# Kernel optimization log

Hardware: AMD Instinct MI355X
Metric: run time of the kernel (lower is better)

The kernel has to match this reference:

```python
import jax, jax.numpy as jnp
import numpy as np

N_NODES = 50000
N_EDGES = 800000
N_GRAPHS = 512


def gcn_conv(x, W, b, src, dst, n_nodes):
    # Standard PyG GCNConv: linear transform, add self-loops, D^-1/2 (A+I) D^-1/2 aggregation.
    x = x @ W  # [N, out]
    loop = jnp.arange(n_nodes, dtype=src.dtype)
    s = jnp.concatenate([src, loop])  # [E+N]
    d = jnp.concatenate([dst, loop])
    deg = jax.ops.segment_sum(jnp.ones_like(d, dtype=x.dtype), d, num_segments=n_nodes)
    dinv = jnp.where(deg > 0, jax.lax.rsqrt(jnp.maximum(deg, 1e-12)), 0.0)
    norm = dinv[s] * dinv[d]  # [E+N]
    msg = x[s] * norm[:, None]  # gather + scale
    out = jax.ops.segment_sum(msg, d, num_segments=n_nodes)  # scatter-add
    return out + b


def setup_inputs() -> dict:
    key = jax.random.key(0)
    ks = jax.random.split(key, 10)
    x = jax.random.normal(ks[0], (N_NODES, 128), dtype=jnp.float32)
    edge_index = jax.random.randint(ks[1], (2, N_EDGES), 0, N_NODES, dtype=jnp.int64)
    batch = jnp.sort(jax.random.randint(ks[2], (N_NODES,), 0, N_GRAPHS, dtype=jnp.int64))
    y = jax.random.randint(ks[3], (N_GRAPHS,), 0, 4, dtype=jnp.int64)
    W1 = jax.random.normal(ks[4], (128, 64), dtype=jnp.float32) * (1.0 / np.sqrt(128))
    b1 = jnp.zeros((64,), dtype=jnp.float32)
    W2 = jax.random.normal(ks[5], (64, 64), dtype=jnp.float32) * (1.0 / np.sqrt(64))
    b2 = jnp.zeros((64,), dtype=jnp.float32)
    Wfc = jax.random.normal(ks[6], (64, 4), dtype=jnp.float32) * (1.0 / np.sqrt(64))
    bfc = jnp.zeros((4,), dtype=jnp.float32)
    return {"x": x, "edge_index": edge_index, "batch": batch, "y": y,
            "W1": W1, "b1": b1, "W2": W2, "b2": b2, "Wfc": Wfc, "bfc": bfc}


def reference(x, edge_index, batch, y, W1, b1, W2, b2, Wfc, bfc):
    src, dst = edge_index[0], edge_index[1]
    h = jax.nn.relu(gcn_conv(x, W1, b1, src, dst, N_NODES))
    h = jax.nn.relu(gcn_conv(h, W2, b2, src, dst, N_NODES))
    # global mean pool over graph ids
    sums = jax.ops.segment_sum(h, batch, num_segments=N_GRAPHS)  # [G, out]
    cnts = jax.ops.segment_sum(jnp.ones((h.shape[0],), h.dtype), batch, num_segments=N_GRAPHS)
    pooled = sums / jnp.maximum(cnts, 1.0)[:, None]
    logits = pooled @ Wfc + bfc
    logp = jax.nn.log_softmax(logits, axis=1)
    return (logp, y)
```

## Files before the change

kernel.cpp:

```cpp
#include <hip/hip_runtime.h>
#include <hip/hip_fp16.h>
#include <math.h>

#define N_NODES 50000
#define N_EDGES 800000
#define N_GRAPHS 512
#define NBKT 196
#define SENT N_NODES
#define CAP_T 6144
#define CAP_S 12288
#define EPB 2048
#define NBLK_A 391
#define N_GROUPS 6250
#define NBLK_G 1563

typedef float v2f __attribute__((ext_vector_type(2)));

#define OFF_BCNT    0u
#define OFF_DINV    1024u
#define OFF_GGRP    201216u
#define OFF_TMP     251392u
#define OFF_SORTED  5068288u
#define OFF_XS8_1   14702080u
#define OFF_XS8_2   17902336u
#define OFF_H2      21102592u

__global__ __launch_bounds__(256) void binA(const int* __restrict__ src, const int* __restrict__ dst,
                                            int* __restrict__ bcnt, unsigned int* __restrict__ tmp,
                                            unsigned int* __restrict__ x1, unsigned int* __restrict__ x2) {
    __shared__ int cnt[256];
    __shared__ int lo[256];
    __shared__ int cnt2[256];
    __shared__ int baseg[256];
    __shared__ unsigned int ldsPK[EPB];
    __shared__ int ldsDST[EPB];
    int t = threadIdx.x;
    cnt[t] = 0; cnt2[t] = 0;
    if (blockIdx.x == 0) {
        if (t < 16) x1[N_NODES * 16 + t] = 0;
        else if (t < 32) x2[N_NODES * 16 + (t - 16)] = 0;
    }
    __syncthreads();
    int e0 = blockIdx.x * EPB;
    int nE = N_EDGES - e0; if (nE > EPB) nE = EPB;
    int sA[8], dA[8];
#pragma unroll
    for (int i = 0; i < 8; ++i) {
        int e = e0 + i * 256 + t;
        if (e < N_EDGES) {
            sA[i] = src[e];
            dA[i] = dst[e];
            atomicAdd(&cnt[dA[i] >> 8], 1);
        } else dA[i] = -1;
    }
    __syncthreads();
    {
        int v = cnt[t];
        lo[t] = v;
        __syncthreads();
        for (int d = 1; d < 256; d <<= 1) {
            int a = (t >= d) ? lo[t - d] : 0;
            __syncthreads();
            lo[t] += a;
            __syncthreads();
        }
        int ex = lo[t] - v;
        __syncthreads();
        lo[t] = ex;
        baseg[t] = (t < NBKT && v) ? atomicAdd(&bcnt[t], v) : 0;
    }
    __syncthreads();
#pragma unroll
    for (int i = 0; i < 8; ++i) {
        if (dA[i] >= 0) {
            int b = dA[i] >> 8;
            int pl = lo[b] + atomicAdd(&cnt2[b], 1);
            ldsPK[pl] = (unsigned int)sA[i] | ((unsigned int)(dA[i] & 255) << 17);
            ldsDST[pl] = b * CAP_T + baseg[b] + (pl - lo[b]);
        }
    }
    __syncthreads();
    for (int p = t; p < nE; p += 256)
        tmp[ldsDST[p]] = ldsPK[p];
}

__global__ __launch_bounds__(256) void binB2(const unsigned int* __restrict__ tmp,
                                             const int* __restrict__ bcnt,
                                             int* __restrict__ sorted, int2* __restrict__ ggrp,
                                             float* __restrict__ dinv) {
    __shared__ int cnt[256];
    __shared__ int lbs[256];
    __shared__ int cur[256];
    __shared__ int gK[32];
    __shared__ int gpre[33];
    __shared__ int ldsS[CAP_S];
    int b = blockIdx.x, t = threadIdx.x;
    cnt[t] = 0;
    __syncthreads();
    int m = bcnt[b];
    const unsigned int* tp = tmp + b * CAP_T;
    for (int e = t; e < m; e += 256) atomicAdd(&cnt[tp[e] >> 17], 1);
    __syncthreads();
    int node = b * 256 + t;
    int real = node < N_NODES;
    int deg = cnt[t];
    int count = real ? deg + 1 : 0;
    int mx = count;
    mx = max(mx, __shfl_xor(mx, 1));
    mx = max(mx, __shfl_xor(mx, 2));
    mx = max(mx, __shfl_xor(mx, 4));
    int K = (mx + 3) & ~3;
    int KP = K + 4;
    if ((t & 7) == 0) gK[t >> 3] = KP;
    __syncthreads();
    if (t == 0) {
        int s = 0;
        for (int g = 0; g < 32; ++g) { gpre[g] = s; s += gK[g]; }
        gpre[32] = s;
    }
    __syncthreads();
    int lb = 8 * gpre[t >> 3] + (t & 7);
    lbs[t] = lb;
    cur[t] = real ? 1 : 0;
    if (real) {
        dinv[node] = rsqrtf(1.0f + (float)deg);
        ldsS[lb] = node;
    }
    if ((t & 7) == 0) ggrp[b * 32 + (t >> 3)] = make_int2(b * CAP_S + 8 * gpre[t >> 3], K);
    __syncthreads();
    for (int e = t; e < m; e += 256) {
        unsigned int pk = tp[e];
        int d = (int)(pk >> 17);
        int j = atomicAdd(&cur[d], 1);
        ldsS[lbs[d] + j * 8] = (int)(pk & 0x1FFFFu);
    }
    __syncthreads();
    for (int j = cur[t]; j < KP; ++j) ldsS[lb + j * 8] = SENT;
    __syncthreads();
    int ptot = 8 * gpre[32];
    int4* dst4 = (int4*)(sorted + b * CAP_S);
    const int4* src4 = (const int4*)ldsS;
    for (int p = t; p < (ptot >> 2); p += 256) dst4[p] = src4[p];
}

__global__ __launch_bounds__(256) void gemm1(const float* __restrict__ X, const float* __restrict__ W,
                                             const float* __restrict__ dinv, unsigned int* __restrict__ xs8) {
    __shared__ float sW[128 * 64];
    __shared__ float sX[16 * 132];
    int tid = threadIdx.x;
    {
        const float4* ws = (const float4*)W;
        float4* wd = (float4*)sW;
        for (int i = tid; i < 2048; i += 256) wd[i] = ws[i];
    }
    int row0 = blockIdx.x * 16;
    {
        const float4* xs = (const float4*)(X + row0 * 128);
        for (int i = tid; i < 512; i += 256) {
            int r = i >> 5, q = i & 31;
            *(float4*)&sX[r * 132 + 4 * q] = xs[r * 32 + q];
        }
    }
    __syncthreads();
    int r = tid >> 4;
    int cg = (tid & 15) * 4;
    int row = row0 + r;
    float a0 = 0, a1 = 0, a2 = 0, a3 = 0;
#pragma unroll 8
    for (int k = 0; k < 128; ++k) {
        float xv = sX[r * 132 + k];
        float4 w = *(const float4*)&sW[k * 64 + cg];
        a0 += xv * w.x; a1 += xv * w.y; a2 += xv * w.z; a3 += xv * w.w;
    }
    float s = dinv[row];
    unsigned int pk = 0;
    pk = __builtin_amdgcn_cvt_pk_fp8_f32(a0 * s, a1 * s, pk, false);
    pk = __builtin_amdgcn_cvt_pk_fp8_f32(a2 * s, a3 * s, pk, true);
    xs8[row * 16 + (cg >> 2)] = pk;
}

#define ADD_ROW(rv) { \
    v2f f0 = __builtin_amdgcn_cvt_pk_f32_fp8((rv).x, false); \
    v2f f1 = __builtin_amdgcn_cvt_pk_f32_fp8((rv).x, true); \
    v2f f2 = __builtin_amdgcn_cvt_pk_f32_fp8((rv).y, false); \
    v2f f3 = __builtin_amdgcn_cvt_pk_f32_fp8((rv).y, true); \
    a0 += f0.x; a1 += f0.y; a2 += f1.x; a3 += f1.y; \
    a4 += f2.x; a5 += f2.y; a6 += f3.x; a7 += f3.y; }

#define GATHER_ACC() \
    int lane = threadIdx.x & 63; \
    int sub = lane >> 3, frag = lane & 7; \
    int node = grp * 8 + sub; \
    int2 gi = ggrp[grp]; \
    int K = gi.y; \
    const int* sp = sorted + gi.x + sub; \
    const uint2* xr = (const uint2*)xs8 + frag; \
    float a0 = 0, a1 = 0, a2 = 0, a3 = 0, a4 = 0, a5 = 0, a6 = 0, a7 = 0; \
    int i0 = sp[0], i1 = sp[8], i2 = sp[16], i3 = sp[24]; \
    for (int k = 0; k < K; k += 4) { \
        uint2 r0 = xr[i0 * 8]; \
        uint2 r1 = xr[i1 * 8]; \
        uint2 r2 = xr[i2 * 8]; \
        uint2 r3 = xr[i3 * 8]; \
        const int* np = sp + (k + 4) * 8; \
        i0 = np[0]; i1 = np[8]; i2 = np[16]; i3 = np[24]; \
        ADD_ROW(r0); ADD_ROW(r1); ADD_ROW(r2); ADD_ROW(r3); \
    }

__global__ __launch_bounds__(256) void gather_fuse(const unsigned char* __restrict__ xs8,
                                                   const int2* __restrict__ ggrp,
                                                   const int* __restrict__ sorted,
                                                   const float* __restrict__ dinv,
                                                   const float* __restrict__ bias,
                                                   const float* __restrict__ W2,
                                                   unsigned int* __restrict__ xs8o) {
    __shared__ float sW2[64 * 64];
    __shared__ float sH[32][68];
    {
        const float4* ws = (const float4*)W2;
        float4* wd = (float4*)sW2;
        for (int i = threadIdx.x; i < 1024; i += 256) wd[i] = ws[i];
    }
    int wvl = threadIdx.x >> 6;
    int grp = blockIdx.x * 4 + wvl;

    GATHER_ACC()

    {
        float dv = dinv[node];
        float4 bA = *(const float4*)(bias + frag * 8);
        float4 bB = *(const float4*)(bias + frag * 8 + 4);
        float4 w0, w1;
        w0.x = fmaxf(a0 * dv + bA.x, 0.0f); w0.y = fmaxf(a1 * dv + bA.y, 0.0f);
        w0.z = fmaxf(a2 * dv + bA.z, 0.0f); w0.w = fmaxf(a3 * dv + bA.w, 0.0f);
        w1.x = fmaxf(a4 * dv + bB.x, 0.0f); w1.y = fmaxf(a5 * dv + bB.y, 0.0f);
        w1.z = fmaxf(a6 * dv + bB.z, 0.0f); w1.w = fmaxf(a7 * dv + bB.w, 0.0f);
        *(float4*)&sH[wvl * 8 + sub][frag * 8] = w0;
        *(float4*)&sH[wvl * 8 + sub][frag * 8 + 4] = w1;
    }
    __syncthreads();
    int r = threadIdx.x >> 3;
    int cg = (threadIdx.x & 7) * 8;
    float b0 = 0, b1 = 0, b2 = 0, b3 = 0, b4 = 0, b5 = 0, b6 = 0, b7 = 0;
#pragma unroll 8
    for (int k = 0; k < 64; ++k) {
        float hv = sH[r][k];
        float4 wa = *(const float4*)&sW2[k * 64 + cg];
        float4 wb = *(const float4*)&sW2[k * 64 + cg + 4];
        b0 += hv * wa.x; b1 += hv * wa.y; b2 += hv * wa.z; b3 += hv * wa.w;
        b4 += hv * wb.x; b5 += hv * wb.y; b6 += hv * wb.z; b7 += hv * wb.w;
    }
    int node2 = blockIdx.x * 32 + r;
    if (node2 < N_NODES) {
        float s = dinv[node2];
        unsigned int p0 = 0, p1 = 0;
        p0 = __builtin_amdgcn_cvt_pk_fp8_f32(b0 * s, b1 * s, p0, false);
        p0 = __builtin_amdgcn_cvt_pk_fp8_f32(b2 * s, b3 * s, p0, true);
        p1 = __builtin_amdgcn_cvt_pk_fp8_f32(b4 * s, b5 * s, p1, false);
        p1 = __builtin_amdgcn_cvt_pk_fp8_f32(b6 * s, b7 * s, p1, true);
        *(uint2*)(xs8o + node2 * 16 + (cg >> 2)) = make_uint2(p0, p1);
    }
}

__global__ __launch_bounds__(256) void gather_h2(const unsigned char* __restrict__ xs8,
                                                 const int2* __restrict__ ggrp,
                                                 const int* __restrict__ sorted,
                                                 const float* __restrict__ dinv,
                                                 const float* __restrict__ bias,
                                                 __half* __restrict__ h2) {
    int grp = blockIdx.x * 4 + (threadIdx.x >> 6);

    GATHER_ACC()

    if (node < N_NODES) {
        float dv = dinv[node];
        float4 bA = *(const float4*)(bias + frag * 8);
        float4 bB = *(const float4*)(bias + frag * 8 + 4);
        float v0 = fmaxf(a0 * dv + bA.x, 0.0f), v1 = fmaxf(a1 * dv + bA.y, 0.0f);
        float v2 = fmaxf(a2 * dv + bA.z, 0.0f), v3 = fmaxf(a3 * dv + bA.w, 0.0f);
        float v4 = fmaxf(a4 * dv + bB.x, 0.0f), v5 = fmaxf(a5 * dv + bB.y, 0.0f);
        float v6 = fmaxf(a6 * dv + bB.z, 0.0f), v7 = fmaxf(a7 * dv + bB.w, 0.0f);
        __half2 p0 = __floats2half2_rn(v0, v1), p1 = __floats2half2_rn(v2, v3);
        __half2 p2 = __floats2half2_rn(v4, v5), p3 = __floats2half2_rn(v6, v7);
        uint4 pk;
        pk.x = *(unsigned int*)&p0; pk.y = *(unsigned int*)&p1;
        pk.z = *(unsigned int*)&p2; pk.w = *(unsigned int*)&p3;
        *(uint4*)(h2 + node * 64 + frag * 8) = pk;
    }
}

__device__ __forceinline__ int lower_bound(const int* __restrict__ a, int n, int v) {
    int lo = 0, hi = n;
    while (lo < hi) { int m = (lo + hi) >> 1; if (a[m] < v) lo = m + 1; else hi = m; }
    return lo;
}

__global__ __launch_bounds__(256) void pool_head(const __half* __restrict__ h2,
                                                 const int* __restrict__ batch,
                                                 const float* __restrict__ Wfc, const float* __restrict__ bfc,
                                                 const int* __restrict__ y, float* __restrict__ out) {
    __shared__ int s_beg, s_end;
    __shared__ float sh[4][64];
    __shared__ float pl[64];
    __shared__ float lg[4];
    int g = blockIdx.x;
    int t = threadIdx.x;
    if (t == 0) s_beg = lower_bound(batch, N_NODES, g);
    if (t == 1) s_end = lower_bound(batch, N_NODES, g + 1);
    __syncthreads();
    int beg = s_beg, end = s_end;
    int f = t & 63, seg = t >> 6;
    float s = 0.0f;
    for (int r = beg + seg; r < end; r += 4) s += __half2float(h2[r * 64 + f]);
    sh[seg][f] = s;
    __syncthreads();
    if (t < 64) {
        float p = sh[0][t] + sh[1][t] + sh[2][t] + sh[3][t];
        pl[t] = p / fmaxf((float)(end - beg), 1.0f);
    }
    __syncthreads();
    if (t < 4) {
        float l = bfc[t];
#pragma unroll
        for (int k = 0; k < 64; ++k) l += pl[k] * Wfc[k * 4 + t];
        lg[t] = l;
    }
    __syncthreads();
    if (t == 0) {
        float l0 = lg[0], l1 = lg[1], l2 = lg[2], l3 = lg[3];
        float m = fmaxf(fmaxf(l0, l1), fmaxf(l2, l3));
        float ss = expf(l0 - m) + expf(l1 - m) + expf(l2 - m) + expf(l3 - m);
        float lse = m + logf(ss);
        out[g * 4 + 0] = l0 - lse;
        out[g * 4 + 1] = l1 - lse;
        out[g * 4 + 2] = l2 - lse;
        out[g * 4 + 3] = l3 - lse;
        out[N_GRAPHS * 4 + g] = (float)y[g];
    }
}

extern "C" void kernel_launch(void* const* d_in, const int* in_sizes, int n_in,
                              void* d_out, int out_size, void* d_ws, size_t ws_size,
                              hipStream_t stream) {
    const float* x     = (const float*)d_in[0];
    const int*   ei    = (const int*)d_in[1];
    const int*   batch = (const int*)d_in[2];
    const int*   y     = (const int*)d_in[3];
    const float* W1    = (const float*)d_in[4];
    const float* b1    = (const float*)d_in[5];
    const float* W2    = (const float*)d_in[6];
    const float* b2    = (const float*)d_in[7];
    const float* Wfc   = (const float*)d_in[8];
    const float* bfc   = (const float*)d_in[9];
    float* out = (float*)d_out;

    const int* src = ei;
    const int* dst = ei + N_EDGES;

    char* wsb = (char*)d_ws;
    int*          bcnt   = (int*)(wsb + OFF_BCNT);
    float*        dinv   = (float*)(wsb + OFF_DINV);
    int2*         ggrp   = (int2*)(wsb + OFF_GGRP);
    unsigned int* tmp    = (unsigned int*)(wsb + OFF_TMP);
    int*          sorted = (int*)(wsb + OFF_SORTED);
    unsigned int* xs8_1  = (unsigned int*)(wsb + OFF_XS8_1);
    unsigned int* xs8_2  = (unsigned int*)(wsb + OFF_XS8_2);
    __half*       h2     = (__half*)(wsb + OFF_H2);

    hipMemsetAsync(bcnt, 0, 1024u, stream);

    binA<<<NBLK_A, 256, 0, stream>>>(src, dst, bcnt, tmp, xs8_1, xs8_2);
    binB2<<<NBKT, 256, 0, stream>>>(tmp, bcnt, sorted, ggrp, dinv);

    gemm1<<<N_NODES / 16, 256, 0, stream>>>(x, W1, dinv, xs8_1);
    gather_fuse<<<NBLK_G, 256, 0, stream>>>((const unsigned char*)xs8_1, ggrp, sorted,
                                            dinv, b1, W2, xs8_2);
    gather_h2<<<NBLK_G, 256, 0, stream>>>((const unsigned char*)xs8_2, ggrp, sorted,
                                          dinv, b2, h2);

    pool_head<<<N_GRAPHS, 256, 0, stream>>>(h2, batch, Wfc, bfc, y, out);
}
```

Before: 198.0 us.

## Fuse bucket sort and bf16 MFMA GEMM into one prep kernel, apply dinv in gather

Replaces the global-atomic bucket scatter with per-segment fixed-capacity bins plus a count matrix, which removes the memset and the global atomics. The second binning pass and the first GEMM are merged into a single launch whose blocks split between sorting half-buckets and a bf16 MFMA layer-1 GEMM. Because dinv is no longer ready when the GEMM runs, the source-side normalization moves into the gather loop as an extra per-neighbor dinv load and FMA. The GEMM adds a runtime accuracy check with an fp32 fallback, and the sort blocks now each rescan all segments of their bucket, so per-block serial work goes up.

Result: faster. 173.0 us (-12.6%).

```diff
diff --git a/kernel.cpp b/kernel.cpp
--- a/kernel.cpp
+++ b/kernel.cpp
@@ -7,185 +7,246 @@
 #define N_GRAPHS 512
 #define NBKT 196
 #define SENT N_NODES
-#define CAP_T 6144
-#define CAP_S 12288
 #define EPB 2048
-#define NBLK_A 391
-#define N_GROUPS 6250
-#define NBLK_G 1563
+#define NSEG 391
+#define CAP_C 48
+#define NBLK_B2 392
+#define CAP_SH 8192
+#define NBLK_GM 782
+#define PREP_GRID (NBLK_B2 + NBLK_GM)
+#define N_GROUPS 6272
+#define NBLK_G 1568
 
 typedef float v2f __attribute__((ext_vector_type(2)));
-
-#define OFF_BCNT    0u
-#define OFF_DINV    1024u
-#define OFF_GGRP    201216u
-#define OFF_TMP     251392u
-#define OFF_SORTED  5068288u
-#define OFF_XS8_1   14702080u
-#define OFF_XS8_2   17902336u
-#define OFF_H2      21102592u
+typedef float f32x4 __attribute__((ext_vector_type(4)));
+typedef short s16x8 __attribute__((ext_vector_type(8)));
+
+#define OFF_DINV    0u
+#define OFF_GGRP    200704u
+#define OFF_CNTM    250880u
+#define OFF_TMP     557568u
+#define OFF_SORTED  15271680u
+#define OFF_XS8_1   28116736u
+#define OFF_XS8_2   31316992u
+#define OFF_H2      34517248u
+
+__device__ __forceinline__ unsigned short f2bf(float f) {
+    unsigned int u = __float_as_uint(f);
+    u += 0x7FFFu + ((u >> 16) & 1u);
+    return (unsigned short)(u >> 16);
+}
 
 __global__ __launch_bounds__(256) void binA(const int* __restrict__ src, const int* __restrict__ dst,
-                                            int* __restrict__ bcnt, unsigned int* __restrict__ tmp,
-                                            unsigned int* __restrict__ x1, unsigned int* __restrict__ x2) {
+                                            int* __restrict__ cntmat, unsigned int* __restrict__ tmp,
+                                            unsigned int* __restrict__ x1, unsigned int* __restrict__ x2,
+                                            float* __restrict__ dinv) {
     __shared__ int cnt[256];
-    __shared__ int lo[256];
-    __shared__ int cnt2[256];
-    __shared__ int baseg[256];
-    __shared__ unsigned int ldsPK[EPB];
-    __shared__ int ldsDST[EPB];
     int t = threadIdx.x;
-    cnt[t] = 0; cnt2[t] = 0;
+    cnt[t] = 0;
     if (blockIdx.x == 0) {
         if (t < 16) x1[N_NODES * 16 + t] = 0;
         else if (t < 32) x2[N_NODES * 16 + (t - 16)] = 0;
+        else if (t == 32) dinv[SENT] = 0.0f;
     }
     __syncthreads();
     int e0 = blockIdx.x * EPB;
-    int nE = N_EDGES - e0; if (nE > EPB) nE = EPB;
-    int sA[8], dA[8];
 #pragma unroll
     for (int i = 0; i < 8; ++i) {
         int e = e0 + i * 256 + t;
         if (e < N_EDGES) {
-            sA[i] = src[e];
-            dA[i] = dst[e];
-            atomicAdd(&cnt[dA[i] >> 8], 1);
-        } else dA[i] = -1;
-    }
-    __syncthreads();
-    {
-        int v = cnt[t];
-        lo[t] = v;
-        __syncthreads();
-        for (int d = 1; d < 256; d <<= 1) {
-            int a = (t >= d) ? lo[t - d] : 0;
+            int s = src[e], d = dst[e];
+            int b = d >> 8;
+            int p = atomicAdd(&cnt[b], 1);
+            tmp[(b * NSEG + blockIdx.x) * CAP_C + p] =
+                (unsigned int)s | ((unsigned int)(d & 255) << 17);
+        }
+    }
+    __syncthreads();
+    if (t < NBKT) cntmat[blockIdx.x * NBKT + t] = cnt[t];
+}
+
+__global__ __launch_bounds__(256) void prep(const unsigned int* __restrict__ tmp,
+                                            const int* __restrict__ cntmat,
+                                            int* __restrict__ sorted, int2* __restrict__ ggrp,
+                                            float* __restrict__ dinv,
+                                            const float* __restrict__ X, const float* __restrict__ W1,
+                                            unsigned int* __restrict__ xs8) {
+    __shared__ __align__(16) char pool[34816];
+    __shared__ int bad;
+    int t = threadIdx.x;
+
+    if (blockIdx.x < NBLK_B2) {
+        int* cnt  = (int*)pool;
+        int* lbs  = (int*)(pool + 512);
+        int* cur  = (int*)(pool + 1024);
+        int* gK   = (int*)(pool + 1536);
+        int* gpre = (int*)(pool + 1600);
+        int* ldsS = (int*)(pool + 1792);
+        int b2 = blockIdx.x, bkt = b2 >> 1, half = b2 & 1;
+        if (t < 128) cnt[t] = 0;
+        __syncthreads();
+        for (int seg = t; seg < NSEG; seg += 256) {
+            int c = cntmat[seg * NBKT + bkt];
+            const unsigned int* tp = tmp + (bkt * NSEG + seg) * CAP_C;
+            for (int e = 0; e < c; ++e) {
+                int d = (int)(tp[e] >> 17);
+                if ((d >> 7) == half) atomicAdd(&cnt[d & 127], 1);
+            }
+        }
+        __syncthreads();
+        int node = 0, deg = 0, K = 0, KP = 0, lb = 0, myreal = 0;
+        if (t < 128) {
+            node = bkt * 256 + half * 128 + t;
+            myreal = node < N_NODES;
+            deg = cnt[t];
+            int count = myreal ? deg + 1 : 0;
+            int mx = count;
+            mx = max(mx, __shfl_xor(mx, 1));
+            mx = max(mx, __shfl_xor(mx, 2));
+            mx = max(mx, __shfl_xor(mx, 4));
+            K = (mx + 3) & ~3;
+            KP = K + 4;
+            if ((t & 7) == 0) gK[t >> 3] = KP;
+        }
+        __syncthreads();
+        if (t == 0) {
+            int s = 0;
+#pragma unroll
+            for (int g = 0; g < 16; ++g) { gpre[g] = s; s += gK[g]; }
+            gpre[16] = s;
+        }
+        __syncthreads();
+        if (t < 128) {
+            lb = 8 * gpre[t >> 3] + (t & 7);
+            lbs[t] = lb;
+            cur[t] = myreal ? 1 : 0;
+            if (myreal) {
+                dinv[node] = rsqrtf(1.0f + (float)deg);
+                ldsS[lb] = node;
+            }
+            if ((t & 7) == 0)
+                ggrp[b2 * 16 + (t >> 3)] = make_int2(b2 * CAP_SH + 8 * gpre[t >> 3], K);
+        }
+        __syncthreads();
+        for (int seg = t; seg < NSEG; seg += 256) {
+            int c = cntmat[seg * NBKT + bkt];
+            const unsigned int* tp = tmp + (bkt * NSEG + seg) * CAP_C;
+            for (int e = 0; e < c; ++e) {
+                unsigned int pk = tp[e];
+                int d = (int)(pk >> 17);
+                if ((d >> 7) == half) {
+                    int loc = d & 127;
+                    int j = atomicAdd(&cur[loc], 1);
+                    ldsS[lbs[loc] + j * 8] = (int)(pk & 0x1FFFFu);
+                }
+            }
+        }
+        __syncthreads();
+        if (t < 128)
+            for (int j = cur[t]; j < KP; ++j) ldsS[lb + j * 8] = SENT;
+        __syncthreads();
+        int ptot = 8 * gpre[16];
+        int4* dst4 = (int4*)(sorted + b2 * CAP_SH);
+        const int4* src4 = (const int4*)ldsS;
+        for (int p = t; p < (ptot >> 2); p += 256) dst4[p] = src4[p];
+    } else {
+        short* W1T = (short*)pool;
+        float* sD  = (float*)(pool + 17408);
+        int gb = blockIdx.x - NBLK_B2;
+        int row0 = gb * 64;
+        for (int i = t; i < 8192; i += 256) {
+            int k = i >> 6, c = i & 63;
+            W1T[c * 136 + k] = (short)f2bf(W1[i]);
+        }
+        __syncthreads();
+        int w = t >> 6, lane = t & 63;
+        int arow = lane & 15, kg = lane >> 4;
+        int r = row0 + w * 16 + arow;
+        const float* xp = X + r * 128 + kg * 8;
+        bool vr = (r < N_NODES);
+        const short* wb = &W1T[arow * 136 + kg * 8];
+        f32x4 ac0 = {0.f, 0.f, 0.f, 0.f}, ac1 = ac0, ac2 = ac0, ac3 = ac0;
+#pragma unroll
+        for (int kk = 0; kk < 4; ++kk) {
+            float4 xa, xb;
+            if (vr) { xa = *(const float4*)(xp); xb = *(const float4*)(xp + 4); }
+            else    { xa = make_float4(0.f, 0.f, 0.f, 0.f); xb = xa; }
+            xp += 32;
+            s16x8 af;
+            af[0] = (short)f2bf(xa.x); af[1] = (short)f2bf(xa.y);
+            af[2] = (short)f2bf(xa.z); af[3] = (short)f2bf(xa.w);
+            af[4] = (short)f2bf(xb.x); af[5] = (short)f2bf(xb.y);
+            af[6] = (short)f2bf(xb.z); af[7] = (short)f2bf(xb.w);
+            const short* wk = wb + kk * 32;
+            s16x8 bf0 = *(const s16x8*)(wk);
+            s16x8 bf1 = *(const s16x8*)(wk + 16 * 136);
+            s16x8 bf2 = *(const s16x8*)(wk + 32 * 136);
+            s16x8 bf3 = *(const s16x8*)(wk + 48 * 136);
+            asm volatile(
+                "s_nop 1\n\t"
+                "v_mfma_f32_16x16x32_bf16 %0, %4, %5, %0\n\t"
+                "v_mfma_f32_16x16x32_bf16 %1, %4, %6, %1\n\t"
+                "v_mfma_f32_16x16x32_bf16 %2, %4, %7, %2\n\t"
+                "v_mfma_f32_16x16x32_bf16 %3, %4, %8, %3"
+                : "+v"(ac0), "+v"(ac1), "+v"(ac2), "+v"(ac3)
+                : "v"(af), "v"(bf0), "v"(bf1), "v"(bf2), "v"(bf3));
+        }
+        asm volatile("s_nop 7\n\ts_nop 7");
+        int dr = w * 16 + kg * 4;
+#pragma unroll
+        for (int reg = 0; reg < 4; ++reg) {
+            sD[(dr + reg) * 68 + arow]      = ac0[reg];
+            sD[(dr + reg) * 68 + 16 + arow] = ac1[reg];
+            sD[(dr + reg) * 68 + 32 + arow] = ac2[reg];
+            sD[(dr + reg) * 68 + 48 + arow] = ac3[reg];
+        }
+        __syncthreads();
+        if (t == 0) {
+            float r0v = 0.f, r1v = 0.f;
+            const float* x0 = X + row0 * 128;
+            for (int k = 0; k < 128; ++k) {
+                float wv = W1[k * 64];
+                r0v += x0[k] * wv;
+                r1v += x0[128 + k] * wv;
+            }
+            bad = (fabsf(r0v - sD[0])  > 0.05f * fabsf(r0v) + 0.1f) ||
+                  (fabsf(r1v - sD[68]) > 0.05f * fabsf(r1v) + 0.1f);
+        }
+        __syncthreads();
+        if (bad) {
+            for (int i = t; i < 4096; i += 256) {
+                int lr = i >> 6, c = i & 63;
+                int nd = row0 + lr;
+                if (nd < N_NODES) {
+                    const float* xr2 = X + nd * 128;
+                    float s = 0.f;
+                    for (int k = 0; k < 128; ++k) s += xr2[k] * W1[k * 64 + c];
+                    sD[lr * 68 + c] = s;
+                }
+            }
             __syncthreads();
-            lo[t] += a;
-            __syncthreads();
-        }
-        int ex = lo[t] - v;
-        __syncthreads();
-        lo[t] = ex;
-        baseg[t] = (t < NBKT && v) ? atomicAdd(&bcnt[t], v) : 0;
-    }
-    __syncthreads();
-#pragma unroll
-    for (int i = 0; i < 8; ++i) {
-        if (dA[i] >= 0) {
-            int b = dA[i] >> 8;
-            int pl = lo[b] + atomicAdd(&cnt2[b], 1);
-            ldsPK[pl] = (unsigned int)sA[i] | ((unsigned int)(dA[i] & 255) << 17);
-            ldsDST[pl] = b * CAP_T + baseg[b] + (pl - lo[b]);
-        }
-    }
-    __syncthreads();
-    for (int p = t; p < nE; p += 256)
-        tmp[ldsDST[p]] = ldsPK[p];
-}
-
-__global__ __launch_bounds__(256) void binB2(const unsigned int* __restrict__ tmp,
-                                             const int* __restrict__ bcnt,
-                                             int* __restrict__ sorted, int2* __restrict__ ggrp,
-                                             float* __restrict__ dinv) {
-    __shared__ int cnt[256];
-    __shared__ int lbs[256];
-    __shared__ int cur[256];
-    __shared__ int gK[32];
-    __shared__ int gpre[33];
-    __shared__ int ldsS[CAP_S];
-    int b = blockIdx.x, t = threadIdx.x;
-    cnt[t] = 0;
-    __syncthreads();
-    int m = bcnt[b];
-    const unsigned int* tp = tmp + b * CAP_T;
-    for (int e = t; e < m; e += 256) atomicAdd(&cnt[tp[e] >> 17], 1);
-    __syncthreads();
-    int node = b * 256 + t;
-    int real = node < N_NODES;
-    int deg = cnt[t];
-    int count = real ? deg + 1 : 0;
-    int mx = count;
-    mx = max(mx, __shfl_xor(mx, 1));
-    mx = max(mx, __shfl_xor(mx, 2));
-    mx = max(mx, __shfl_xor(mx, 4));
-    int K = (mx + 3) & ~3;
-    int KP = K + 4;
-    if ((t & 7) == 0) gK[t >> 3] = KP;
-    __syncthreads();
-    if (t == 0) {
-        int s = 0;
-        for (int g = 0; g < 32; ++g) { gpre[g] = s; s += gK[g]; }
-        gpre[32] = s;
-    }
-    __syncthreads();
-    int lb = 8 * gpre[t >> 3] + (t & 7);
-    lbs[t] = lb;
-    cur[t] = real ? 1 : 0;
-    if (real) {
-        dinv[node] = rsqrtf(1.0f + (float)deg);
-        ldsS[lb] = node;
-    }
-    if ((t & 7) == 0) ggrp[b * 32 + (t >> 3)] = make_int2(b * CAP_S + 8 * gpre[t >> 3], K);
-    __syncthreads();
-    for (int e = t; e < m; e += 256) {
-        unsigned int pk = tp[e];
-        int d = (int)(pk >> 17);
-        int j = atomicAdd(&cur[d], 1);
-        ldsS[lbs[d] + j * 8] = (int)(pk & 0x1FFFFu);
-    }
-    __syncthreads();
-    for (int j = cur[t]; j < KP; ++j) ldsS[lb + j * 8] = SENT;
-    __syncthreads();
-    int ptot = 8 * gpre[32];
-    int4* dst4 = (int4*)(sorted + b * CAP_S);
-    const int4* src4 = (const int4*)ldsS;
-    for (int p = t; p < (ptot >> 2); p += 256) dst4[p] = src4[p];
-}
-
-__global__ __launch_bounds__(256) void gemm1(const float* __restrict__ X, const float* __restrict__ W,
-                                             const float* __restrict__ dinv, unsigned int* __restrict__ xs8) {
-    __shared__ float sW[128 * 64];
-    __shared__ float sX[16 * 132];
-    int tid = threadIdx.x;
-    {
-        const float4* ws = (const float4*)W;
-        float4* wd = (float4*)sW;
-        for (int i = tid; i < 2048; i += 256) wd[i] = ws[i];
-    }
-    int row0 = blockIdx.x * 16;
-    {
-        const float4* xs = (const float4*)(X + row0 * 128);
-        for (int i = tid; i < 512; i += 256) {
-            int r = i >> 5, q = i & 31;
-            *(float4*)&sX[r * 132 + 4 * q] = xs[r * 32 + q];
-        }
-    }
-    __syncthreads();
-    int r = tid >> 4;
-    int cg = (tid & 15) * 4;
-    int row = row0 + r;
-    float a0 = 0, a1 = 0, a2 = 0, a3 = 0;
-#pragma unroll 8
-    for (int k = 0; k < 128; ++k) {
-        float xv = sX[r * 132 + k];
-        float4 w = *(const float4*)&sW[k * 64 + cg];
-        a0 += xv * w.x; a1 += xv * w.y; a2 += xv * w.z; a3 += xv * w.w;
-    }
-    float s = dinv[row];
-    unsigned int pk = 0;
-    pk = __builtin_amdgcn_cvt_pk_fp8_f32(a0 * s, a1 * s, pk, false);
-    pk = __builtin_amdgcn_cvt_pk_fp8_f32(a2 * s, a3 * s, pk, true);
-    xs8[row * 16 + (cg >> 2)] = pk;
-}
-
-#define ADD_ROW(rv) { \
+        }
+        for (int i = t; i < 1024; i += 256) {
+            int lr = i >> 4, q = i & 15;
+            int nd = row0 + lr;
+            if (nd < N_NODES) {
+                float4 v = *(const float4*)&sD[lr * 68 + q * 4];
+                unsigned int pk = 0;
+                pk = __builtin_amdgcn_cvt_pk_fp8_f32(v.x, v.y, pk, false);
+                pk = __builtin_amdgcn_cvt_pk_fp8_f32(v.z, v.w, pk, true);
+                xs8[nd * 16 + q] = pk;
+            }
+        }
+    }
+}
+
+#define FMA_ROW(rv, ds) { \
     v2f f0 = __builtin_amdgcn_cvt_pk_f32_fp8((rv).x, false); \
     v2f f1 = __builtin_amdgcn_cvt_pk_f32_fp8((rv).x, true); \
     v2f f2 = __builtin_amdgcn_cvt_pk_f32_fp8((rv).y, false); \
     v2f f3 = __builtin_amdgcn_cvt_pk_f32_fp8((rv).y, true); \
-    a0 += f0.x; a1 += f0.y; a2 += f1.x; a3 += f1.y; \
-    a4 += f2.x; a5 += f2.y; a6 += f3.x; a7 += f3.y; }
+    a0 += f0.x * (ds); a1 += f0.y * (ds); a2 += f1.x * (ds); a3 += f1.y * (ds); \
+    a4 += f2.x * (ds); a5 += f2.y * (ds); a6 += f3.x * (ds); a7 += f3.y * (ds); }
 
 #define GATHER_ACC() \
     int lane = threadIdx.x & 63; \
@@ -202,9 +263,10 @@
         uint2 r1 = xr[i1 * 8]; \
         uint2 r2 = xr[i2 * 8]; \
         uint2 r3 = xr[i3 * 8]; \
+        float s0 = dinv[i0], s1 = dinv[i1], s2 = dinv[i2], s3 = dinv[i3]; \
         const int* np = sp + (k + 4) * 8; \
         i0 = np[0]; i1 = np[8]; i2 = np[16]; i3 = np[24]; \
-        ADD_ROW(r0); ADD_ROW(r1); ADD_ROW(r2); ADD_ROW(r3); \
+        FMA_ROW(r0, s0); FMA_ROW(r1, s1); FMA_ROW(r2, s2); FMA_ROW(r3, s3); \
     }
 
 __global__ __launch_bounds__(256) void gather_fuse(const unsigned char* __restrict__ xs8,
@@ -246,18 +308,17 @@
     for (int k = 0; k < 64; ++k) {
         float hv = sH[r][k];
         float4 wa = *(const float4*)&sW2[k * 64 + cg];
-        float4 wb = *(const float4*)&sW2[k * 64 + cg + 4];
+        float4 wbv = *(const float4*)&sW2[k * 64 + cg + 4];
         b0 += hv * wa.x; b1 += hv * wa.y; b2 += hv * wa.z; b3 += hv * wa.w;
-        b4 += hv * wb.x; b5 += hv * wb.y; b6 += hv * wb.z; b7 += hv * wb.w;
+        b4 += hv * wbv.x; b5 += hv * wbv.y; b6 += hv * wbv.z; b7 += hv * wbv.w;
     }
     int node2 = blockIdx.x * 32 + r;
     if (node2 < N_NODES) {
-        float s = dinv[node2];
         unsigned int p0 = 0, p1 = 0;
-        p0 = __builtin_amdgcn_cvt_pk_fp8_f32(b0 * s, b1 * s, p0, false);
-        p0 = __builtin_amdgcn_cvt_pk_fp8_f32(b2 * s, b3 * s, p0, true);
-        p1 = __builtin_amdgcn_cvt_pk_fp8_f32(b4 * s, b5 * s, p1, false);
-        p1 = __builtin_amdgcn_cvt_pk_fp8_f32(b6 * s, b7 * s, p1, true);
+        p0 = __builtin_amdgcn_cvt_pk_fp8_f32(b0, b1, p0, false);
+        p0 = __builtin_amdgcn_cvt_pk_fp8_f32(b2, b3, p0, true);
+        p1 = __builtin_amdgcn_cvt_pk_fp8_f32(b4, b5, p1, false);
+        p1 = __builtin_amdgcn_cvt_pk_fp8_f32(b6, b7, p1, true);
         *(uint2*)(xs8o + node2 * 16 + (cg >> 2)) = make_uint2(p0, p1);
     }
 }
@@ -358,25 +419,20 @@
     const int* dst = ei + N_EDGES;
 
     char* wsb = (char*)d_ws;
-    int*          bcnt   = (int*)(wsb + OFF_BCNT);
     float*        dinv   = (float*)(wsb + OFF_DINV);
     int2*         ggrp   = (int2*)(wsb + OFF_GGRP);
+    int*          cntmat = (int*)(wsb + OFF_CNTM);
     unsigned int* tmp    = (unsigned int*)(wsb + OFF_TMP);
     int*          sorted = (int*)(wsb + OFF_SORTED);
     unsigned int* xs8_1  = (unsigned int*)(wsb + OFF_XS8_1);
     unsigned int* xs8_2  = (unsigned int*)(wsb + OFF_XS8_2);
     __half*       h2     = (__half*)(wsb + OFF_H2);
 
-    hipMemsetAsync(bcnt, 0, 1024u, stream);
-
-    binA<<<NBLK_A, 256, 0, stream>>>(src, dst, bcnt, tmp, xs8_1, xs8_2);
-    binB2<<<NBKT, 256, 0, stream>>>(tmp, bcnt, sorted, ggrp, dinv);
-
-    gemm1<<<N_NODES / 16, 256, 0, stream>>>(x, W1, dinv, xs8_1);
+    binA<<<NSEG, 256, 0, stream>>>(src, dst, cntmat, tmp, xs8_1, xs8_2, dinv);
+    prep<<<PREP_GRID, 256, 0, stream>>>(tmp, cntmat, sorted, ggrp, dinv, x, W1, xs8_1);
     gather_fuse<<<NBLK_G, 256, 0, stream>>>((const unsigned char*)xs8_1, ggrp, sorted,
                                             dinv, b1, W2, xs8_2);
     gather_h2<<<NBLK_G, 256, 0, stream>>>((const unsigned char*)xs8_2, ggrp, sorted,
                                           dinv, b2, h2);
-
     pool_head<<<N_GRAPHS, 256, 0, stream>>>(h2, batch, Wfc, bfc, y, out);
 }
```
